# Kernel tuning notes

Hardware: AMD Instinct MI355X
Metric: run time of the kernel (lower is better)

The kernel has to match this reference:

```python
import jax, jax.numpy as jnp
import numpy as np

N_NODES = 50000
N_EDGES = 800000
F_IN, HID, CLS = 128, 128, 64
DELTA = 3.0


def setup_inputs() -> dict:
    key = jax.random.key(0)
    ks = jax.random.split(key, 16)
    x = jax.random.normal(ks[0], (N_NODES, F_IN), jnp.float32)
    src = jax.random.randint(ks[1], (N_EDGES,), 0, N_NODES, jnp.int64)
    dst = jax.random.randint(ks[2], (N_EDGES,), 0, N_NODES, jnp.int64)
    dims = [(F_IN, HID), (HID, HID), (HID, CLS)]
    inp = {"x": x, "src": src, "dst": dst}
    k = 3
    for i, (din, dout) in enumerate(dims):
        inp[f"M{i}_w"] = jax.random.normal(ks[k], (2 * din, din), jnp.float32) * 0.05; k += 1
        inp[f"M{i}_b"] = jnp.zeros((din,), jnp.float32)
        inp[f"U{i}_w"] = jax.random.normal(ks[k], (10 * din, dout), jnp.float32) * 0.05; k += 1
        inp[f"U{i}_b"] = jnp.zeros((dout,), jnp.float32)
    return inp


def _pna_layer(h, src, dst, deg, logd, Mw, Mb, Uw, Ub):
    # message: per-edge linear on concat(src feat, dst feat)  [E, 2*din] @ [2*din, din]
    msg = jnp.concatenate([h[src], h[dst]], axis=1) @ Mw + Mb  # [E, din]
    n = h.shape[0]
    cnt = deg[:, None]                                          # [N, 1]
    has_nbr = cnt > 0
    mean = jax.ops.segment_sum(msg, dst, num_segments=n) / jnp.maximum(cnt, 1.0)
    mn = jax.ops.segment_min(msg, dst, num_segments=n)
    mx = jax.ops.segment_max(msg, dst, num_segments=n)
    mn = jnp.where(has_nbr, mn, 0.0)
    mx = jnp.where(has_nbr, mx, 0.0)
    agg = jnp.concatenate([mean, mn, mx], axis=1)               # [N, 3*din]
    amp = (logd / DELTA)[:, None]                               # amplification scaler
    att = (DELTA / jnp.maximum(logd, 1e-6))[:, None]            # attenuation scaler
    h_neigh = jnp.concatenate([agg, agg * amp, agg * att], axis=1)  # [N, 9*din]
    return jnp.concatenate([h, h_neigh], axis=1) @ Uw + Ub      # [N, dout]


def reference(x, src, dst, M0_w, M0_b, U0_w, U0_b, M1_w, M1_b, U1_w, U1_b, M2_w, M2_b, U2_w, U2_b):
    n = x.shape[0]
    deg = jax.ops.segment_sum(jnp.ones_like(dst, dtype=x.dtype), dst, num_segments=n)
    logd = jnp.log(deg + 1.0)
    params = [(M0_w, M0_b, U0_w, U0_b), (M1_w, M1_b, U1_w, U1_b), (M2_w, M2_b, U2_w, U2_b)]
    h = x
    for i, (Mw, Mb, Uw, Ub) in enumerate(params):
        h = _pna_layer(h, src, dst, deg, logd, Mw, Mb, Uw, Ub)
        if i != len(params) - 1:
            h = jax.nn.relu(h)
    return h
```

## Files before the change

kernel.cpp:

```cpp
#include <hip/hip_runtime.h>
#include <math.h>

#define N_NODES 50000
#define N_EDGES 800000
#define DIN 128
#define NB_SCAN ((N_NODES + 255) / 256)

typedef unsigned short u16;
typedef unsigned int u32;
typedef short short8 __attribute__((ext_vector_type(8)));
typedef float f32x4 __attribute__((ext_vector_type(4)));

__device__ __forceinline__ u16 f2bf(float x) {
  u32 u = __float_as_uint(x);
  u32 r = (u + 0x7FFFu + ((u >> 16) & 1u)) >> 16;
  return (u16)r;
}
__device__ __forceinline__ float bf2f(u16 h) { return __uint_as_float(((u32)h) << 16); }
__device__ __forceinline__ u32 pack2bf(float x, float y) {
  return (u32)f2bf(x) | ((u32)f2bf(y) << 16);
}

__device__ __forceinline__ f32x4 mfma_bf16(short8 a, short8 b, f32x4 c) {
  return __builtin_amdgcn_mfma_f32_16x16x32_bf16(a, b, c, 0, 0, 0);
}

#define SWZ(row, byt) ((row) * 128 + ((byt) ^ (((row) & 7) << 4)))


__global__ void k_deg(const int* __restrict__ dst, int* __restrict__ deg) {
  int e = blockIdx.x * blockDim.x + threadIdx.x;
  if (e < N_EDGES) atomicAdd(&deg[dst[e]], 1);
}

__global__ void k_scan_local(const int* __restrict__ deg, int* __restrict__ excl,
                             int* __restrict__ bsum) {
  __shared__ int sm[256];
  int tid = threadIdx.x;
  int i = blockIdx.x * 256 + tid;
  int v = (i < N_NODES) ? deg[i] : 0;
  sm[tid] = v;
  __syncthreads();
  for (int off = 1; off < 256; off <<= 1) {
    int t = (tid >= off) ? sm[tid - off] : 0;
    __syncthreads();
    sm[tid] += t;
    __syncthreads();
  }
  if (i < N_NODES) excl[i] = sm[tid] - v;
  if (tid == 255) bsum[blockIdx.x] = sm[255];
}

__global__ void k_scan_bsum(const int* __restrict__ bsum, int* __restrict__ boff,
                            int* __restrict__ row_off) {
  __shared__ int sm[256];
  int tid = threadIdx.x;
  int v = (tid < NB_SCAN) ? bsum[tid] : 0;
  sm[tid] = v;
  __syncthreads();
  for (int off = 1; off < 256; off <<= 1) {
    int t = (tid >= off) ? sm[tid - off] : 0;
    __syncthreads();
    sm[tid] += t;
    __syncthreads();
  }
  if (tid < NB_SCAN) boff[tid] = sm[tid] - v;
  if (tid == 255) row_off[N_NODES] = sm[255];
}

__global__ void k_scan_add(const int* __restrict__ excl, const int* __restrict__ boff,
                           int* __restrict__ row_off) {
  int i = blockIdx.x * 256 + threadIdx.x;
  if (i < N_NODES) row_off[i] = excl[i] + boff[i >> 8];
}

__global__ void k_node_init(const int* __restrict__ deg, const int* __restrict__ row_off,
                            int* __restrict__ cursor, float* __restrict__ amp,
                            float* __restrict__ att) {
  int v = blockIdx.x * blockDim.x + threadIdx.x;
  if (v >= N_NODES) return;
  cursor[v] = row_off[v];
  float d = (float)deg[v];
  float logd = logf(d + 1.0f);
  amp[v] = logd / 3.0f;
  att[v] = 3.0f / fmaxf(logd, 1e-6f);
}

__global__ void k_fill(const int* __restrict__ src, const int* __restrict__ dst,
                       int* __restrict__ cursor, int* __restrict__ nbr) {
  int e = blockIdx.x * blockDim.x + threadIdx.x;
  if (e >= N_EDGES) return;
  int slot = atomicAdd(&cursor[dst[e]], 1);
  nbr[slot] = src[e];
}


__global__ void k_prep_ab(const float* __restrict__ Mw, const float* __restrict__ Mb,
                          u16* __restrict__ Th, u16* __restrict__ Tl,
                          float* __restrict__ bias_ab) {
  int j = blockIdx.x;
  int k = threadIdx.x;
  float w = (j < 128) ? Mw[k * 128 + j] : Mw[(128 + k) * 128 + (j - 128)];
  u16 hi = f2bf(w);
  u16 lo = f2bf(w - bf2f(hi));
  Th[j * 128 + k] = hi;
  Tl[j * 128 + k] = lo;
  if (k == 0) bias_ab[j] = (j < 128) ? 0.f : Mb[j - 128];
}

__global__ void k_prep_u(const float* __restrict__ Uw, u16* __restrict__ Th,
                         u16* __restrict__ Tl, int Nout) {
  int k = blockIdx.x * 256 + threadIdx.x;
  int j = blockIdx.y;
  int p = blockIdx.z;
  if (p > 0 && k < 128) return;
  int srow = (p == 0) ? k : 512 + 384 * (p - 1) + (k - 128);
  float w = Uw[(size_t)srow * Nout + j];
  u16 hi = f2bf(w);
  u16 lo = f2bf(w - bf2f(hi));
  size_t idx = ((size_t)p * Nout + j) * 512 + k;
  Th[idx] = hi;
  Tl[idx] = lo;
}


__global__ void k_pack_x(const float* __restrict__ x, u16* __restrict__ Xh,
                         u16* __restrict__ Xl) {
  int i = blockIdx.x * 256 + threadIdx.x;
  if (i >= N_NODES * DIN) return;
  int g = i >> 7, c = i & 127;
  float v = x[i];
  u16 hi = f2bf(v);
  Xh[(size_t)g * 512 + c] = hi;
  Xl[(size_t)g * 128 + c] = f2bf(v - bf2f(hi));
}


__global__ __launch_bounds__(256) void k_ab_gemm(
    const u16* __restrict__ Xh, const u16* __restrict__ Xl,
    const u16* __restrict__ WTh, const u16* __restrict__ WTl,
    const float* __restrict__ bias, u16* __restrict__ ABa, float* __restrict__ ABb) {
  __shared__ __align__(16) u16 Ah[128 * 64];
  __shared__ __align__(16) u16 Al[128 * 64];
  __shared__ __align__(16) u16 Bh[128 * 64];
  __shared__ __align__(16) u16 Bl[128 * 64];

  const int tid = threadIdx.x;
  const int row0 = blockIdx.x * 128;
  const int col0 = blockIdx.y * 128;
  const int lane = tid & 63;
  const int wave = tid >> 6;
  const int wrow = (wave >> 1) * 64;
  const int wcol = (wave & 1) * 64;

  f32x4 acc[4][4];
  const f32x4 zero4 = {0.f, 0.f, 0.f, 0.f};
#pragma unroll
  for (int i = 0; i < 4; ++i)
#pragma unroll
    for (int n = 0; n < 4; ++n) acc[i][n] = zero4;

  for (int k0 = 0; k0 < 128; k0 += 64) {
    __syncthreads();
#pragma unroll
    for (int r = 0; r < 4; ++r) {
      int op = r * 256 + tid;
      int m = op >> 3, ch = op & 7;
      int g = row0 + m;
      uint4 hv = {0u, 0u, 0u, 0u}, lv = {0u, 0u, 0u, 0u};
      if (g < N_NODES) {
        hv = *(const uint4*)(Xh + (size_t)g * 512 + k0 + ch * 8);
        lv = *(const uint4*)(Xl + (size_t)g * 128 + k0 + ch * 8);
      }
      int ad = SWZ(m, ch * 16);
      *(uint4*)((char*)Ah + ad) = hv;
      *(uint4*)((char*)Al + ad) = lv;
    }
#pragma unroll
    for (int r = 0; r < 4; ++r) {
      int op = r * 256 + tid;
      int c = op >> 3, sl = op & 7;
      int bd = SWZ(c, sl * 16);
      *(uint4*)((char*)Bh + bd) = *(const uint4*)(WTh + (size_t)(col0 + c) * 128 + k0 + sl * 8);
      *(uint4*)((char*)Bl + bd) = *(const uint4*)(WTl + (size_t)(col0 + c) * 128 + k0 + sl * 8);
    }
    __syncthreads();
#pragma unroll
    for (int kk = 0; kk < 2; ++kk) {
      const int kb = kk * 64 + (lane >> 4) * 16;
      short8 a_h[4], a_l[4];
#pragma unroll
      for (int i = 0; i < 4; ++i) {
        int rr = wrow + i * 16 + (lane & 15);
        a_h[i] = *(const short8*)((const char*)Ah + SWZ(rr, kb));
        a_l[i] = *(const short8*)((const char*)Al + SWZ(rr, kb));
      }
#pragma unroll
      for (int n = 0; n < 4; ++n) {
        int cc = wcol + n * 16 + (lane & 15);
        short8 b_h = *(const short8*)((const char*)Bh + SWZ(cc, kb));
        short8 b_l = *(const short8*)((const char*)Bl + SWZ(cc, kb));
#pragma unroll
        for (int i = 0; i < 4; ++i) {
          acc[i][n] = mfma_bf16(a_h[i], b_h, acc[i][n]);
          acc[i][n] = mfma_bf16(a_h[i], b_l, acc[i][n]);
          acc[i][n] = mfma_bf16(a_l[i], b_h, acc[i][n]);
        }
      }
    }
  }
#pragma unroll
  for (int i = 0; i < 4; ++i) {
#pragma unroll
    for (int n = 0; n < 4; ++n) {
      int gr0 = row0 + wrow + i * 16 + (lane >> 4) * 4;
      int gc = col0 + wcol + n * 16 + (lane & 15);
#pragma unroll
      for (int q = 0; q < 4; ++q) {
        int gr = gr0 + q;
        if (gr >= N_NODES) continue;
        float v = acc[i][n][q];
        if (gc < 128) ABa[(size_t)gr * 128 + gc] = f2bf(v);
        else ABb[(size_t)gr * 128 + (gc - 128)] = v + bias[gc];
      }
    }
  }
}


template <int BN, int LAST>
__global__ __launch_bounds__(256, 2) void k_u_fused(
    const u16* __restrict__ Xh, const u16* __restrict__ Xl,
    const u16* __restrict__ UTh, const u16* __restrict__ UTl,
    const float* __restrict__ Ub, const float* __restrict__ amp,
    const float* __restrict__ att, u16* __restrict__ XhW, u16* __restrict__ XlW,
    float* __restrict__ outF, int Nout) {
  __shared__ __align__(16) u16 Ah[128 * 64];
  __shared__ __align__(16) u16 Al[128 * 64];
  __shared__ __align__(16) u16 Bh[BN * 64];
  __shared__ __align__(16) u16 Bl[BN * 64];

  const int tid = threadIdx.x;
  const int row0 = blockIdx.x * 128;
  const int lane = tid & 63;
  const int wave = tid >> 6;
  const int wrow = (wave >> 1) * 64;
  const int wcol = (wave & 1) * (BN / 2);
  constexpr int NREP = BN / 32;

  f32x4 acc_t[4][NREP], acc_p[4][NREP];
  const f32x4 zero4 = {0.f, 0.f, 0.f, 0.f};
#pragma unroll
  for (int i = 0; i < 4; ++i)
#pragma unroll
    for (int n = 0; n < NREP; ++n) acc_t[i][n] = zero4;

  for (int span = 0; span < 3; ++span) {
    const u16* BTh = UTh + (size_t)span * Nout * 512;
    const u16* BTl = UTl + (size_t)span * Nout * 512;
    const int kbeg = (span == 0) ? 0 : 128;
#pragma unroll
    for (int i = 0; i < 4; ++i)
#pragma unroll
      for (int n = 0; n < NREP; ++n) acc_p[i][n] = zero4;

    for (int k0 = kbeg; k0 < 512; k0 += 64) {
      const bool hstep = (k0 < 128);
      __syncthreads();
#pragma unroll
      for (int r = 0; r < 4; ++r) {
        int op = r * 256 + tid;
        int m = op >> 3, ch = op & 7;
        int g = row0 + m;
        int ad = SWZ(m, ch * 16);
        uint4 hv = {0u, 0u, 0u, 0u};
        if (g < N_NODES) hv = *(const uint4*)(Xh + (size_t)g * 512 + k0 + ch * 8);
        *(uint4*)((char*)Ah + ad) = hv;
        if (hstep) {
          uint4 lv = {0u, 0u, 0u, 0u};
          if (g < N_NODES) lv = *(const uint4*)(Xl + (size_t)g * 128 + k0 + ch * 8);
          *(uint4*)((char*)Al + ad) = lv;
        }
      }
#pragma unroll
      for (int r = 0; r < NREP; ++r) {
        int op = r * 256 + tid;
        int c = op >> 3, sl = op & 7;
        int bd = SWZ(c, sl * 16);
        *(uint4*)((char*)Bh + bd) = *(const uint4*)(BTh + (size_t)c * 512 + k0 + sl * 8);
        *(uint4*)((char*)Bl + bd) = *(const uint4*)(BTl + (size_t)c * 512 + k0 + sl * 8);
      }
      __syncthreads();
#pragma unroll
      for (int kk = 0; kk < 2; ++kk) {
        const int kb = kk * 64 + (lane >> 4) * 16;
        short8 a_h[4], a_l[4];
#pragma unroll
        for (int i = 0; i < 4; ++i) {
          int rr = wrow + i * 16 + (lane & 15);
          a_h[i] = *(const short8*)((const char*)Ah + SWZ(rr, kb));
          if (hstep) a_l[i] = *(const short8*)((const char*)Al + SWZ(rr, kb));
        }
#pragma unroll
        for (int n = 0; n < NREP; ++n) {
          int cc = wcol + n * 16 + (lane & 15);
          short8 b_h = *(const short8*)((const char*)Bh + SWZ(cc, kb));
          short8 b_l = *(const short8*)((const char*)Bl + SWZ(cc, kb));
#pragma unroll
          for (int i = 0; i < 4; ++i) {
            acc_p[i][n] = mfma_bf16(a_h[i], b_h, acc_p[i][n]);
            acc_p[i][n] = mfma_bf16(a_h[i], b_l, acc_p[i][n]);
            if (hstep) acc_p[i][n] = mfma_bf16(a_l[i], b_h, acc_p[i][n]);
          }
        }
      }
    }
    if (span == 0) {
#pragma unroll
      for (int i = 0; i < 4; ++i)
#pragma unroll
        for (int n = 0; n < NREP; ++n) acc_t[i][n] += acc_p[i][n];
    } else {
      const float* sc = (span == 1) ? amp : att;
#pragma unroll
      for (int i = 0; i < 4; ++i) {
        int gr0 = row0 + wrow + i * 16 + (lane >> 4) * 4;
        f32x4 sv = *(const f32x4*)(sc + gr0);
#pragma unroll
        for (int n = 0; n < NREP; ++n)
#pragma unroll
          for (int q = 0; q < 4; ++q) acc_t[i][n][q] += sv[q] * acc_p[i][n][q];
      }
    }
  }
#pragma unroll
  for (int i = 0; i < 4; ++i) {
#pragma unroll
    for (int n = 0; n < NREP; ++n) {
      int gr0 = row0 + wrow + i * 16 + (lane >> 4) * 4;
      int gc = wcol + n * 16 + (lane & 15);
      float b = Ub[gc];
#pragma unroll
      for (int q = 0; q < 4; ++q) {
        int gr = gr0 + q;
        if (gr >= N_NODES) continue;
        float v = acc_t[i][n][q] + b;
        if (LAST) {
          outF[(size_t)gr * 64 + gc] = v;
        } else {
          float t = fmaxf(v, 0.f);
          u16 hi = f2bf(t);
          XhW[(size_t)gr * 512 + gc] = hi;
          XlW[(size_t)gr * 128 + gc] = f2bf(t - bf2f(hi));
        }
      }
    }
  }
}


__global__ __launch_bounds__(256) void k_agg(const u16* __restrict__ ABa,
                                             const float* __restrict__ ABb,
                                             const int* __restrict__ row_off,
                                             const int* __restrict__ nbr,
                                             u16* __restrict__ XhDst) {
  int v = blockIdx.x * 4 + (threadIdx.x >> 6);
  int lane = threadIdx.x & 63;
  if (v >= N_NODES) return;
  int beg = row_off[v], end = row_off[v + 1];
  const u32* A32 = (const u32*)ABa;
  float sx = 0.f, sy = 0.f;
  float mnx = 3.4e38f, mny = 3.4e38f;
  float mxx = -3.4e38f, mxy = -3.4e38f;
  int i = beg;
#define ACC(w)                                              \
  {                                                         \
    float ax = bf2f((u16)(w)), ay = bf2f((u16)((w) >> 16)); \
    sx += ax; sy += ay;                                     \
    mnx = fminf(mnx, ax); mny = fminf(mny, ay);             \
    mxx = fmaxf(mxx, ax); mxy = fmaxf(mxy, ay);             \
  }
  for (; i + 4 <= end; i += 4) {
    int s0 = nbr[i], s1 = nbr[i + 1], s2 = nbr[i + 2], s3 = nbr[i + 3];
    u32 w0 = A32[(size_t)s0 * 64 + lane];
    u32 w1 = A32[(size_t)s1 * 64 + lane];
    u32 w2 = A32[(size_t)s2 * 64 + lane];
    u32 w3 = A32[(size_t)s3 * 64 + lane];
    ACC(w0) ACC(w1) ACC(w2) ACC(w3)
  }
  for (; i < end; ++i) {
    u32 w = A32[(size_t)nbr[i] * 64 + lane];
    ACC(w)
  }
#undef ACC
  int d = end - beg;
  int c = lane * 2;
  float2 b = *(const float2*)&ABb[(size_t)v * 128 + c];
  float mex, mey, mix, miy, max_, may_;
  if (d > 0) {
    float inv = 1.f / (float)d;
    mex = sx * inv + b.x; mey = sy * inv + b.y;
    mix = mnx + b.x; miy = mny + b.y;
    max_ = mxx + b.x; may_ = mxy + b.y;
  } else {
    mex = mey = mix = miy = max_ = may_ = 0.f;
  }
  u16* xr = XhDst + (size_t)v * 512 + 128 + c;
  *(u32*)(xr)       = pack2bf(mex, mey);
  *(u32*)(xr + 128) = pack2bf(mix, miy);
  *(u32*)(xr + 256) = pack2bf(max_, may_);
}


extern "C" void kernel_launch(void* const* d_in, const int* in_sizes, int n_in,
                              void* d_out, int out_size, void* d_ws, size_t ws_size,
                              hipStream_t stream) {
  const float* x   = (const float*)d_in[0];
  const int*   src = (const int*)d_in[1];
  const int*   dst = (const int*)d_in[2];
  const float* Mw[3] = {(const float*)d_in[3], (const float*)d_in[7],  (const float*)d_in[11]};
  const float* Mb[3] = {(const float*)d_in[4], (const float*)d_in[8],  (const float*)d_in[12]};
  const float* Uw[3] = {(const float*)d_in[5], (const float*)d_in[9],  (const float*)d_in[13]};
  const float* Ub[3] = {(const float*)d_in[6], (const float*)d_in[10], (const float*)d_in[14]};
  float* out = (float*)d_out;

  char* ws = (char*)d_ws;
  size_t o = 0;
  auto alloc = [&](size_t bytes) -> char* {
    o = (o + 255) & ~(size_t)255;
    char* p = ws + o;
    o += bytes;
    return p;
  };
  int*   deg_i   = (int*)alloc((size_t)N_NODES * 4);
  int*   row_off = (int*)alloc((size_t)(N_NODES + 1) * 4);
  int*   excl    = (int*)alloc((size_t)N_NODES * 4);
  int*   bsum    = (int*)alloc((size_t)NB_SCAN * 4);
  int*   boff    = (int*)alloc((size_t)NB_SCAN * 4);
  int*   cursor  = (int*)alloc((size_t)N_NODES * 4);
  float* amp     = (float*)alloc((size_t)N_NODES * 4);
  float* att     = (float*)alloc((size_t)N_NODES * 4);
  int*   nbr     = (int*)alloc((size_t)N_EDGES * 4);
  u16*   Xh0     = (u16*)alloc((size_t)N_NODES * 512 * 2);
  u16*   Xl0     = (u16*)alloc((size_t)N_NODES * 128 * 2);
  u16*   Xh1     = (u16*)alloc((size_t)N_NODES * 512 * 2);
  u16*   Xl1     = (u16*)alloc((size_t)N_NODES * 128 * 2);
  u16*   ABa     = (u16*)alloc((size_t)N_NODES * 128 * 2);
  float* ABb     = (float*)alloc((size_t)N_NODES * 128 * 4);
  u16*   WabTh[3]; u16* WabTl[3]; float* bias_ab[3];
  u16*   UTh[3];   u16* UTl[3];
  const int Nouts[3] = {128, 128, 64};
  for (int L = 0; L < 3; ++L) {
    WabTh[L] = (u16*)alloc((size_t)256 * 128 * 2);
    WabTl[L] = (u16*)alloc((size_t)256 * 128 * 2);
    bias_ab[L] = (float*)alloc(256 * 4);
    UTh[L] = (u16*)alloc((size_t)3 * Nouts[L] * 512 * 2);
    UTl[L] = (u16*)alloc((size_t)3 * Nouts[L] * 512 * 2);
  }

  hipMemsetAsync(deg_i, 0, (size_t)N_NODES * 4, stream);
  k_deg<<<(N_EDGES + 255) / 256, 256, 0, stream>>>(dst, deg_i);
  k_scan_local<<<NB_SCAN, 256, 0, stream>>>(deg_i, excl, bsum);
  k_scan_bsum<<<1, 256, 0, stream>>>(bsum, boff, row_off);
  k_scan_add<<<NB_SCAN, 256, 0, stream>>>(excl, boff, row_off);
  k_node_init<<<(N_NODES + 255) / 256, 256, 0, stream>>>(deg_i, row_off, cursor, amp, att);
  k_fill<<<(N_EDGES + 255) / 256, 256, 0, stream>>>(src, dst, cursor, nbr);

  for (int L = 0; L < 3; ++L) {
    k_prep_ab<<<256, 128, 0, stream>>>(Mw[L], Mb[L], WabTh[L], WabTl[L], bias_ab[L]);
    k_prep_u<<<dim3(2, Nouts[L], 3), 256, 0, stream>>>(Uw[L], UTh[L], UTl[L], Nouts[L]);
  }
  k_pack_x<<<(N_NODES * DIN + 255) / 256, 256, 0, stream>>>(x, Xh0, Xl0);

  const int MT = (N_NODES + 127) / 128;
  u16* XhIn[3] = {Xh0, Xh1, Xh0};
  u16* XlIn[3] = {Xl0, Xl1, Xl0};
  u16* XhOut[3] = {Xh1, Xh0, nullptr};
  u16* XlOut[3] = {Xl1, Xl0, nullptr};

  for (int L = 0; L < 3; ++L) {
    k_ab_gemm<<<dim3(MT, 2), 256, 0, stream>>>(XhIn[L], XlIn[L], WabTh[L], WabTl[L],
                                               bias_ab[L], ABa, ABb);
    k_agg<<<(N_NODES + 3) / 4, 256, 0, stream>>>(ABa, ABb, row_off, nbr, XhIn[L]);
    if (L < 2) {
      k_u_fused<128, 0><<<dim3(MT, 1), 256, 0, stream>>>(
          XhIn[L], XlIn[L], UTh[L], UTl[L], Ub[L], amp, att,
          XhOut[L], XlOut[L], nullptr, Nouts[L]);
    } else {
      k_u_fused<64, 1><<<dim3(MT, 1), 256, 0, stream>>>(
          XhIn[L], XlIn[L], UTh[L], UTl[L], Ub[L], amp, att,
          nullptr, nullptr, out, Nouts[L]);
    }
  }
}
```

Before: 697.0 us.

## Split GEMM column tiles and merge amp/att spans into one shared A pass

The edge-message GEMM and the node-update GEMM now use half-width column tiles, which doubles the grid in the column dimension and sets launch bounds to target three blocks per CU. The update kernel no longer streams the aggregated features three times, once per span. It loads each A tile once and accumulates the amp-scaled and att-scaled products into two separate accumulators from B tiles loaded side by side, with the shared-memory buffers aliased through a single array. The goal is more parallelism and less redundant A traffic. In exchange, the A tiles are re-read by each column block, and the extra accumulators add register pressure.

```diff
diff --git a/kernel.cpp b/kernel.cpp
--- a/kernel.cpp
+++ b/kernel.cpp
@@ -136,29 +136,29 @@
 }
 
 
-__global__ __launch_bounds__(256) void k_ab_gemm(
+__global__ __launch_bounds__(256, 3) void k_ab_gemm(
     const u16* __restrict__ Xh, const u16* __restrict__ Xl,
     const u16* __restrict__ WTh, const u16* __restrict__ WTl,
     const float* __restrict__ bias, u16* __restrict__ ABa, float* __restrict__ ABb) {
   __shared__ __align__(16) u16 Ah[128 * 64];
   __shared__ __align__(16) u16 Al[128 * 64];
-  __shared__ __align__(16) u16 Bh[128 * 64];
-  __shared__ __align__(16) u16 Bl[128 * 64];
+  __shared__ __align__(16) u16 Bh[64 * 64];
+  __shared__ __align__(16) u16 Bl[64 * 64];
 
   const int tid = threadIdx.x;
   const int row0 = blockIdx.x * 128;
-  const int col0 = blockIdx.y * 128;
+  const int col0 = blockIdx.y * 64;
   const int lane = tid & 63;
   const int wave = tid >> 6;
   const int wrow = (wave >> 1) * 64;
-  const int wcol = (wave & 1) * 64;
-
-  f32x4 acc[4][4];
+  const int wcol = (wave & 1) * 32;
+
+  f32x4 acc[4][2];
   const f32x4 zero4 = {0.f, 0.f, 0.f, 0.f};
 #pragma unroll
   for (int i = 0; i < 4; ++i)
 #pragma unroll
-    for (int n = 0; n < 4; ++n) acc[i][n] = zero4;
+    for (int n = 0; n < 2; ++n) acc[i][n] = zero4;
 
   for (int k0 = 0; k0 < 128; k0 += 64) {
     __syncthreads();
@@ -177,7 +177,7 @@
       *(uint4*)((char*)Al + ad) = lv;
     }
 #pragma unroll
-    for (int r = 0; r < 4; ++r) {
+    for (int r = 0; r < 2; ++r) {
       int op = r * 256 + tid;
       int c = op >> 3, sl = op & 7;
       int bd = SWZ(c, sl * 16);
@@ -196,7 +196,7 @@
         a_l[i] = *(const short8*)((const char*)Al + SWZ(rr, kb));
       }
 #pragma unroll
-      for (int n = 0; n < 4; ++n) {
+      for (int n = 0; n < 2; ++n) {
         int cc = wcol + n * 16 + (lane & 15);
         short8 b_h = *(const short8*)((const char*)Bh + SWZ(cc, kb));
         short8 b_l = *(const short8*)((const char*)Bl + SWZ(cc, kb));
@@ -212,7 +212,7 @@
 #pragma unroll
   for (int i = 0; i < 4; ++i) {
 #pragma unroll
-    for (int n = 0; n < 4; ++n) {
+    for (int n = 0; n < 2; ++n) {
       int gr0 = row0 + wrow + i * 16 + (lane >> 4) * 4;
       int gc = col0 + wcol + n * 16 + (lane & 15);
 #pragma unroll
@@ -229,122 +229,166 @@
 
 
 template <int BN, int LAST>
-__global__ __launch_bounds__(256, 2) void k_u_fused(
+__global__ __launch_bounds__(256, 3) void k_u_fused(
     const u16* __restrict__ Xh, const u16* __restrict__ Xl,
     const u16* __restrict__ UTh, const u16* __restrict__ UTl,
     const float* __restrict__ Ub, const float* __restrict__ amp,
     const float* __restrict__ att, u16* __restrict__ XhW, u16* __restrict__ XlW,
     float* __restrict__ outF, int Nout) {
-  __shared__ __align__(16) u16 Ah[128 * 64];
-  __shared__ __align__(16) u16 Al[128 * 64];
-  __shared__ __align__(16) u16 Bh[BN * 64];
-  __shared__ __align__(16) u16 Bl[BN * 64];
+  constexpr int NREP = BN / 32;
+  constexpr int BE = BN * 64;
+  constexpr int L1E = 16384 + 2 * BE;
+  constexpr int L2E = 8192 + 4 * BE;
+  constexpr int LDSE = (L1E > L2E) ? L1E : L2E;
+  __shared__ __align__(16) u16 LDS[LDSE];
+  u16* Ah  = LDS;
+  u16* Al  = LDS + 8192;
+  u16* B0h = LDS + 16384;
+  u16* B0l = LDS + 16384 + BE;
+  u16* B1h = LDS + 8192;
+  u16* B1l = LDS + 8192 + BE;
+  u16* B2h = LDS + 8192 + 2 * BE;
+  u16* B2l = LDS + 8192 + 3 * BE;
 
   const int tid = threadIdx.x;
   const int row0 = blockIdx.x * 128;
+  const int col0 = blockIdx.y * BN;
   const int lane = tid & 63;
   const int wave = tid >> 6;
   const int wrow = (wave >> 1) * 64;
   const int wcol = (wave & 1) * (BN / 2);
-  constexpr int NREP = BN / 32;
-
-  f32x4 acc_t[4][NREP], acc_p[4][NREP];
+
+  const u16* U0h = UTh + (size_t)col0 * 512;
+  const u16* U0l = UTl + (size_t)col0 * 512;
+  const u16* U1h = UTh + (size_t)(Nout + col0) * 512;
+  const u16* U1l = UTl + (size_t)(Nout + col0) * 512;
+  const u16* U2h = UTh + (size_t)(2 * Nout + col0) * 512;
+  const u16* U2l = UTl + (size_t)(2 * Nout + col0) * 512;
+
+  f32x4 acc_t[4][NREP], acc_p1[4][NREP], acc_p2[4][NREP];
   const f32x4 zero4 = {0.f, 0.f, 0.f, 0.f};
 #pragma unroll
   for (int i = 0; i < 4; ++i)
 #pragma unroll
-    for (int n = 0; n < NREP; ++n) acc_t[i][n] = zero4;
-
-  for (int span = 0; span < 3; ++span) {
-    const u16* BTh = UTh + (size_t)span * Nout * 512;
-    const u16* BTl = UTl + (size_t)span * Nout * 512;
-    const int kbeg = (span == 0) ? 0 : 128;
-#pragma unroll
-    for (int i = 0; i < 4; ++i)
-#pragma unroll
-      for (int n = 0; n < NREP; ++n) acc_p[i][n] = zero4;
-
-    for (int k0 = kbeg; k0 < 512; k0 += 64) {
-      const bool hstep = (k0 < 128);
-      __syncthreads();
-#pragma unroll
-      for (int r = 0; r < 4; ++r) {
-        int op = r * 256 + tid;
-        int m = op >> 3, ch = op & 7;
-        int g = row0 + m;
-        int ad = SWZ(m, ch * 16);
-        uint4 hv = {0u, 0u, 0u, 0u};
-        if (g < N_NODES) hv = *(const uint4*)(Xh + (size_t)g * 512 + k0 + ch * 8);
-        *(uint4*)((char*)Ah + ad) = hv;
-        if (hstep) {
-          uint4 lv = {0u, 0u, 0u, 0u};
-          if (g < N_NODES) lv = *(const uint4*)(Xl + (size_t)g * 128 + k0 + ch * 8);
-          *(uint4*)((char*)Al + ad) = lv;
+    for (int n = 0; n < NREP; ++n) {
+      acc_t[i][n] = zero4; acc_p1[i][n] = zero4; acc_p2[i][n] = zero4;
+    }
+
+  for (int k0 = 0; k0 < 512; k0 += 64) {
+    const bool hstep = (k0 < 128);
+    __syncthreads();
+#pragma unroll
+    for (int r = 0; r < 4; ++r) {
+      int op = r * 256 + tid;
+      int m = op >> 3, ch = op & 7;
+      int g = row0 + m;
+      int ad = SWZ(m, ch * 16);
+      uint4 hv = {0u, 0u, 0u, 0u};
+      if (g < N_NODES) hv = *(const uint4*)(Xh + (size_t)g * 512 + k0 + ch * 8);
+      *(uint4*)((char*)Ah + ad) = hv;
+      if (hstep) {
+        uint4 lv = {0u, 0u, 0u, 0u};
+        if (g < N_NODES) lv = *(const uint4*)(Xl + (size_t)g * 128 + k0 + ch * 8);
+        *(uint4*)((char*)Al + ad) = lv;
+      }
+    }
+#pragma unroll
+    for (int r = 0; r < NREP; ++r) {
+      int op = r * 256 + tid;
+      int c = op >> 3, sl = op & 7;
+      int bd = SWZ(c, sl * 16);
+      *(uint4*)((char*)B0h + bd) = *(const uint4*)(U0h + (size_t)c * 512 + k0 + sl * 8);
+      *(uint4*)((char*)B0l + bd) = *(const uint4*)(U0l + (size_t)c * 512 + k0 + sl * 8);
+    }
+    __syncthreads();
+#pragma unroll
+    for (int kk = 0; kk < 2; ++kk) {
+      const int kb = kk * 64 + (lane >> 4) * 16;
+      short8 a_h[4], a_l[4];
+#pragma unroll
+      for (int i = 0; i < 4; ++i) {
+        int rr = wrow + i * 16 + (lane & 15);
+        a_h[i] = *(const short8*)((const char*)Ah + SWZ(rr, kb));
+        if (hstep) a_l[i] = *(const short8*)((const char*)Al + SWZ(rr, kb));
+      }
+#pragma unroll
+      for (int n = 0; n < NREP; ++n) {
+        int cc = wcol + n * 16 + (lane & 15);
+        short8 b_h = *(const short8*)((const char*)B0h + SWZ(cc, kb));
+        short8 b_l = *(const short8*)((const char*)B0l + SWZ(cc, kb));
+#pragma unroll
+        for (int i = 0; i < 4; ++i) {
+          acc_t[i][n] = mfma_bf16(a_h[i], b_h, acc_t[i][n]);
+          acc_t[i][n] = mfma_bf16(a_h[i], b_l, acc_t[i][n]);
+          if (hstep) acc_t[i][n] = mfma_bf16(a_l[i], b_h, acc_t[i][n]);
         }
       }
-#pragma unroll
-      for (int r = 0; r < NREP; ++r) {
-        int op = r * 256 + tid;
-        int c = op >> 3, sl = op & 7;
-        int bd = SWZ(c, sl * 16);
-        *(uint4*)((char*)Bh + bd) = *(const uint4*)(BTh + (size_t)c * 512 + k0 + sl * 8);
-        *(uint4*)((char*)Bl + bd) = *(const uint4*)(BTl + (size_t)c * 512 + k0 + sl * 8);
-      }
-      __syncthreads();
-#pragma unroll
-      for (int kk = 0; kk < 2; ++kk) {
-        const int kb = kk * 64 + (lane >> 4) * 16;
-        short8 a_h[4], a_l[4];
+    }
+  }
+
+  for (int k0 = 128; k0 < 512; k0 += 64) {
+    __syncthreads();
+#pragma unroll
+    for (int r = 0; r < 4; ++r) {
+      int op = r * 256 + tid;
+      int m = op >> 3, ch = op & 7;
+      int g = row0 + m;
+      uint4 hv = {0u, 0u, 0u, 0u};
+      if (g < N_NODES) hv = *(const uint4*)(Xh + (size_t)g * 512 + k0 + ch * 8);
+      *(uint4*)((char*)Ah + SWZ(m, ch * 16)) = hv;
+    }
+#pragma unroll
+    for (int r = 0; r < NREP; ++r) {
+      int op = r * 256 + tid;
+      int c = op >> 3, sl = op & 7;
+      int bd = SWZ(c, sl * 16);
+      *(uint4*)((char*)B1h + bd) = *(const uint4*)(U1h + (size_t)c * 512 + k0 + sl * 8);
+      *(uint4*)((char*)B1l + bd) = *(const uint4*)(U1l + (size_t)c * 512 + k0 + sl * 8);
+      *(uint4*)((char*)B2h + bd) = *(const uint4*)(U2h + (size_t)c * 512 + k0 + sl * 8);
+      *(uint4*)((char*)B2l + bd) = *(const uint4*)(U2l + (size_t)c * 512 + k0 + sl * 8);
+    }
+    __syncthreads();
+#pragma unroll
+    for (int kk = 0; kk < 2; ++kk) {
+      const int kb = kk * 64 + (lane >> 4) * 16;
+      short8 a_h[4];
+#pragma unroll
+      for (int i = 0; i < 4; ++i) {
+        int rr = wrow + i * 16 + (lane & 15);
+        a_h[i] = *(const short8*)((const char*)Ah + SWZ(rr, kb));
+      }
+#pragma unroll
+      for (int n = 0; n < NREP; ++n) {
+        int cc = wcol + n * 16 + (lane & 15);
+        short8 b1h = *(const short8*)((const char*)B1h + SWZ(cc, kb));
+        short8 b1l = *(const short8*)((const char*)B1l + SWZ(cc, kb));
+        short8 b2h = *(const short8*)((const char*)B2h + SWZ(cc, kb));
+        short8 b2l = *(const short8*)((const char*)B2l + SWZ(cc, kb));
 #pragma unroll
         for (int i = 0; i < 4; ++i) {
-          int rr = wrow + i * 16 + (lane & 15);
-          a_h[i] = *(const short8*)((const char*)Ah + SWZ(rr, kb));
-          if (hstep) a_l[i] = *(const short8*)((const char*)Al + SWZ(rr, kb));
+          acc_p1[i][n] = mfma_bf16(a_h[i], b1h, acc_p1[i][n]);
+          acc_p1[i][n] = mfma_bf16(a_h[i], b1l, acc_p1[i][n]);
+          acc_p2[i][n] = mfma_bf16(a_h[i], b2h, acc_p2[i][n]);
+          acc_p2[i][n] = mfma_bf16(a_h[i], b2l, acc_p2[i][n]);
         }
-#pragma unroll
-        for (int n = 0; n < NREP; ++n) {
-          int cc = wcol + n * 16 + (lane & 15);
-          short8 b_h = *(const short8*)((const char*)Bh + SWZ(cc, kb));
-          short8 b_l = *(const short8*)((const char*)Bl + SWZ(cc, kb));
-#pragma unroll
-          for (int i = 0; i < 4; ++i) {
-            acc_p[i][n] = mfma_bf16(a_h[i], b_h, acc_p[i][n]);
-            acc_p[i][n] = mfma_bf16(a_h[i], b_l, acc_p[i][n]);
-            if (hstep) acc_p[i][n] = mfma_bf16(a_l[i], b_h, acc_p[i][n]);
-          }
-        }
-      }
-    }
-    if (span == 0) {
-#pragma unroll
-      for (int i = 0; i < 4; ++i)
-#pragma unroll
-        for (int n = 0; n < NREP; ++n) acc_t[i][n] += acc_p[i][n];
-    } else {
-      const float* sc = (span == 1) ? amp : att;
-#pragma unroll
-      for (int i = 0; i < 4; ++i) {
-        int gr0 = row0 + wrow + i * 16 + (lane >> 4) * 4;
-        f32x4 sv = *(const f32x4*)(sc + gr0);
-#pragma unroll
-        for (int n = 0; n < NREP; ++n)
-#pragma unroll
-          for (int q = 0; q < 4; ++q) acc_t[i][n][q] += sv[q] * acc_p[i][n][q];
-      }
-    }
-  }
+      }
+    }
+  }
+
 #pragma unroll
   for (int i = 0; i < 4; ++i) {
+    int gr0 = row0 + wrow + i * 16 + (lane >> 4) * 4;
+    f32x4 a1 = *(const f32x4*)(amp + gr0);
+    f32x4 a2 = *(const f32x4*)(att + gr0);
 #pragma unroll
     for (int n = 0; n < NREP; ++n) {
-      int gr0 = row0 + wrow + i * 16 + (lane >> 4) * 4;
-      int gc = wcol + n * 16 + (lane & 15);
+      int gc = col0 + wcol + n * 16 + (lane & 15);
       float b = Ub[gc];
 #pragma unroll
       for (int q = 0; q < 4; ++q) {
         int gr = gr0 + q;
         if (gr >= N_NODES) continue;
-        float v = acc_t[i][n][q] + b;
+        float v = acc_t[i][n][q] + a1[q] * acc_p1[i][n][q] + a2[q] * acc_p2[i][n][q] + b;
         if (LAST) {
           outF[(size_t)gr * 64 + gc] = v;
         } else {
@@ -479,15 +523,15 @@
   u16* XlOut[3] = {Xl1, Xl0, nullptr};
 
   for (int L = 0; L < 3; ++L) {
-    k_ab_gemm<<<dim3(MT, 2), 256, 0, stream>>>(XhIn[L], XlIn[L], WabTh[L], WabTl[L],
+    k_ab_gemm<<<dim3(MT, 4), 256, 0, stream>>>(XhIn[L], XlIn[L], WabTh[L], WabTl[L],
                                                bias_ab[L], ABa, ABb);
     k_agg<<<(N_NODES + 3) / 4, 256, 0, stream>>>(ABa, ABb, row_off, nbr, XhIn[L]);
     if (L < 2) {
-      k_u_fused<128, 0><<<dim3(MT, 1), 256, 0, stream>>>(
+      k_u_fused<64, 0><<<dim3(MT, 2), 256, 0, stream>>>(
           XhIn[L], XlIn[L], UTh[L], UTl[L], Ub[L], amp, att,
           XhOut[L], XlOut[L], nullptr, Nouts[L]);
     } else {
-      k_u_fused<64, 1><<<dim3(MT, 1), 256, 0, stream>>>(
+      k_u_fused<32, 1><<<dim3(MT, 2), 256, 0, stream>>>(
           XhIn[L], XlIn[L], UTh[L], UTl[L], Ub[L], amp, att,
           nullptr, nullptr, out, Nouts[L]);
     }
```

Result: faster. 680.4 us (-2.4%).
